# Kernel optimization log

Measured on AMD Instinct MI355X. Metric: run time of the kernel, lower is better.

Reference implementation:

```python
import jax, jax.numpy as jnp
import numpy as np

OUT, IN = 14336, 4096          # Llama FFN up-projection
N = OUT * IN                   # total quantized elements
NB = N // 64                   # NF4 blocks (blocksize 64)
NG = N // 256                  # double-quant groups (group size 256)
B = 32                         # batch rows


def setup_inputs() -> dict:
    key = jax.random.key(0)
    ks = jax.random.split(key, 7)
    x = jax.random.normal(ks[0], (B, IN), dtype=jnp.float16)
    # packed bytes: two 4-bit nibbles per byte (values 0..255)
    packed = jax.random.randint(ks[1], (N // 2,), 0, 256, dtype=jnp.int32)
    absmax = jax.random.uniform(ks[2], (NB,), dtype=jnp.float32)                     # per-block absmax
    code = jax.random.uniform(ks[3], (NB,), jnp.float32, minval=0.5, maxval=1.5)     # per-block code scale
    offset = jax.random.uniform(ks[4], (NB,), jnp.float32, minval=0.0, maxval=8.0)   # per-block offset
    g_absmax = jax.random.uniform(ks[5], (NG,), jnp.float32, minval=0.5, maxval=1.5) # nested (state2) absmax
    g_code = jax.random.uniform(ks[6], (NG,), jnp.float32, minval=0.5, maxval=1.5)   # nested (state2) code
    return {"x": x, "packed": packed, "absmax": absmax, "code": code,
            "offset": offset, "g_absmax": g_absmax, "g_code": g_code}


def _dequantize_nf4(packed, absmax, code, offset, g_absmax, g_code):
    # Unpack nibbles: even element = low nibble (byte & 15), odd = high nibble (byte >> 4)
    low = packed & 15
    high = packed >> 4
    nib = jnp.stack([low, high], axis=-1).reshape(-1).astype(jnp.float32)  # [N]
    # Nested (double) dequantization scales, matching the Triton kernel:
    # combined_scale = (absmax / code) * (g_absmax / g_code)
    block_scale = absmax / code                      # [NB]
    group_scale = g_absmax / g_code                  # [NG]
    cs_block = block_scale * jnp.repeat(group_scale, 64 * 4 // 64)  # each group spans 4 blocks -> [NB]
    cs = jnp.repeat(cs_block, 64)                    # per-element combined scale [N]
    off = jnp.repeat(offset, 64)                     # per-element offset [N]
    # dequantized = nibble * cs - offset * cs (as written in the kernel), stored as fp16
    deq = (nib * cs - off * cs).astype(jnp.float16)
    return deq.reshape(OUT, IN)


def reference(x, packed, absmax, code, offset, g_absmax, g_code):
    W = _dequantize_nf4(packed, absmax, code, offset, g_absmax, g_code)  # [OUT, IN] fp16
    return x @ W.T                                                        # [B, OUT] fp16
```

## Files before the change

### kernel.cpp

```cpp
#include <hip/hip_runtime.h>
#include <hip/hip_bf16.h>


#define OUT_D 14336
#define IN_D  4096
#define B_D   32
#define KSPLIT 8
#define KRANGE (IN_D / KSPLIT)
#define KC 64
#define CHUNKS (KRANGE / KC)
#define NB (OUT_D * IN_D / 64)
#define SZ_X (B_D * IN_D)

typedef __attribute__((ext_vector_type(4))) float f32x4;
typedef __attribute__((ext_vector_type(2))) float f32x2;
typedef __attribute__((ext_vector_type(4))) int   i32x4;
typedef __bf16 bf16x8 __attribute__((ext_vector_type(8)));
using u16 = unsigned short;

typedef const __attribute__((address_space(1))) void* gas1_t;
typedef __attribute__((address_space(3))) void* las3_t;

__device__ __forceinline__ void gll16(const void* g, void* l) {
    __builtin_amdgcn_global_load_lds((gas1_t)g, (las3_t)l, 16, 0, 0);
}

__global__ __launch_bounds__(256) void pre_kernel(
    const float* __restrict__ x,
    const float* __restrict__ absmax, const float* __restrict__ code,
    const float* __restrict__ offset,
    const float* __restrict__ g_absmax, const float* __restrict__ g_code,
    u16* __restrict__ xb, f32x2* __restrict__ csn)
{
    const int i = blockIdx.x * 256 + threadIdx.x;
    float am = absmax[i], cd = code[i], of = offset[i];
    float ga = g_absmax[i >> 2], gc = g_code[i >> 2];
    float cs = (am * ga) / (cd * gc);
    f32x2 v; v.x = cs; v.y = -of * cs;
    csn[i] = v;
    if (i < SZ_X) {
        __bf16 h = (__bf16)x[i];
        xb[i] = __builtin_bit_cast(u16, h);
    }
}

__global__ __launch_bounds__(256, 3) void nf4_main(
    const u16* __restrict__ xb,
    const int* __restrict__ packed,
    const f32x2* __restrict__ csn,
    float* __restrict__ part)
{
    __shared__ u16 xs[B_D][512];
    __shared__ int wb[3][32][32];

    const int t      = threadIdx.x;
    const int o_base = blockIdx.x * 32;
    const int kz     = blockIdx.y;

    const int wave = t >> 6, lane = t & 63;
    const int m_base = (wave & 1) * 16, n_base = (wave >> 1) * 16;
    const int frow = lane & 15, q = lane >> 4;
    const int rown = n_base + frow;
    const int rowa = m_base + frow;

    #pragma unroll
    for (int j = 0; j < 8; ++j) {
        int slot = t + j * 256;
        int r = slot >> 6, c = slot & 63;
        bf16x8 v = *reinterpret_cast<const bf16x8*>(xb + r * IN_D + kz * KRANGE + c * 8);
        *reinterpret_cast<bf16x8*>(&xs[r][(c ^ (r & 7)) * 8]) = v;
    }

    f32x4 scp[4];
    {
        const f32x4* sp = reinterpret_cast<const f32x4*>(
            csn + (o_base + rown) * 64 + kz * CHUNKS);
        scp[0] = sp[0]; scp[1] = sp[1]; scp[2] = sp[2]; scp[3] = sp[3];
    }
    __builtin_amdgcn_sched_barrier(0);

    const int srow = t >> 3;
    const int scol = (t & 7) ^ (srow & 7);
    const int* gsrc = packed + (o_base + srow) * (IN_D / 2)
                             + kz * (KRANGE / 2) + scol * 4;

    gll16(gsrc + 0 * 32, &wb[0][wave * 8][0]);
    gll16(gsrc + 1 * 32, &wb[1][wave * 8][0]);

    f32x4 acc = {0.f, 0.f, 0.f, 0.f};

    #pragma unroll
    for (int C = 0; C < CHUNKS; ++C) {
        if (C == 0)               asm volatile("s_waitcnt vmcnt(1) lgkmcnt(0)" ::: "memory");
        else if (C < CHUNKS - 1)  asm volatile("s_waitcnt vmcnt(1)" ::: "memory");
        else                      asm volatile("s_waitcnt vmcnt(0)" ::: "memory");
        __builtin_amdgcn_s_barrier();
        __builtin_amdgcn_sched_barrier(0);

        if (C + 2 < CHUNKS)
            gll16(gsrc + (C + 2) * 32, &wb[(C + 2) % 3][wave * 8][0]);

        const int buf = C % 3;
        const float cs  = scp[C >> 1][(C & 1) * 2];
        const float noc = scp[C >> 1][(C & 1) * 2 + 1];

        #pragma unroll
        for (int s = 0; s < 2; ++s) {
            i32x4 braw = *reinterpret_cast<const i32x4*>(
                &wb[buf][rown][(((s * 4 + q) ^ (rown & 7)) * 4)]);
            int ca = C * 8 + s * 4 + q;
            bf16x8 a = *reinterpret_cast<const bf16x8*>(
                &xs[rowa][(ca ^ (rowa & 7)) * 8]);
            bf16x8 b;
            #pragma unroll
            for (int w = 0; w < 4; ++w) {
                int ww = braw[w];
                b[2 * w]     = (__bf16)fmaf((float)(ww & 15),        cs, noc);
                b[2 * w + 1] = (__bf16)fmaf((float)((ww >> 4) & 15), cs, noc);
            }
            acc = __builtin_amdgcn_mfma_f32_16x16x32_bf16(a, b, acc, 0, 0, 0);
        }
    }

    float* pp = part + (size_t)kz * (B_D * OUT_D);
    const int oc = o_base + n_base + frow;
    const int r0 = m_base + q * 4;
    #pragma unroll
    for (int i = 0; i < 4; ++i)
        pp[(r0 + i) * OUT_D + oc] = acc[i];
}

__global__ __launch_bounds__(256) void reduce_kernel(
    const float* __restrict__ part, float* __restrict__ out)
{
    const int i = (blockIdx.x * 256 + threadIdx.x) * 4;
    f32x4 s = *reinterpret_cast<const f32x4*>(part + i);
    #pragma unroll
    for (int k = 1; k < KSPLIT; ++k) {
        f32x4 v = *reinterpret_cast<const f32x4*>(
            part + (size_t)k * (B_D * OUT_D) + i);
        s[0] += v[0]; s[1] += v[1]; s[2] += v[2]; s[3] += v[3];
    }
    *reinterpret_cast<f32x4*>(out + i) = s;
}

extern "C" void kernel_launch(void* const* d_in, const int* in_sizes, int n_in,
                              void* d_out, int out_size, void* d_ws, size_t ws_size,
                              hipStream_t stream) {
    const void* px = nullptr;
    const void* ppk = nullptr;
    const void* trio[3] = {nullptr, nullptr, nullptr};
    const void* pair[2] = {nullptr, nullptr};
    int ntrio = 0, npair = 0;
    const int SZ_PK  = OUT_D * (IN_D / 2);
    const int SZ_NB  = NB;
    const int SZ_NG  = OUT_D * (IN_D / 256);
    for (int i = 0; i < n_in; ++i) {
        int s = in_sizes[i];
        if (s == SZ_X) px = d_in[i];
        else if (s == SZ_PK) ppk = d_in[i];
        else if (s == SZ_NB) { if (ntrio < 3) trio[ntrio++] = d_in[i]; }
        else if (s == SZ_NG) { if (npair < 2) pair[npair++] = d_in[i]; }
    }
    if (!px || !ppk || ntrio != 3 || npair != 2) {
        px = d_in[0]; ppk = d_in[1];
        trio[0] = d_in[2]; trio[1] = d_in[3]; trio[2] = d_in[4];
        pair[0] = d_in[5]; pair[1] = d_in[6];
    }

    char* ws = (char*)d_ws;
    u16*   xb   = (u16*)ws;
    f32x2* csn  = (f32x2*)(ws + 262144);
    float* part = (float*)(ws + 262144 + (size_t)NB * 8);

    pre_kernel<<<dim3(NB / 256), dim3(256), 0, stream>>>(
        (const float*)px,
        (const float*)trio[0], (const float*)trio[1], (const float*)trio[2],
        (const float*)pair[0], (const float*)pair[1],
        xb, csn);

    nf4_main<<<dim3(OUT_D / 32, KSPLIT), dim3(256), 0, stream>>>(
        xb, (const int*)ppk, csn, part);

    reduce_kernel<<<dim3(B_D * OUT_D / 4 / 256), dim3(256), 0, stream>>>(
        part, (float*)d_out);
}
```

Before: 47.91 us.

## Reduce K-split to 2 with atomic output and larger weight chunks

Lowers the K-split from 8 to 2 and raises the chunk size to 256, so each block streams bigger weight tiles through a triple-buffered LDS pipeline. The x operand now comes straight from global/L2 into registers rather than being staged in LDS. The partial-sum buffer and the separate reduce kernel are removed in favour of a memset plus float atomicAdd into the output. This cuts the partial-buffer write and read traffic and one launch. In exchange the grid drops to 896 blocks, which may leave the GPU underfilled, and the result can vary with atomic ordering.

```diff
diff --git a/kernel.cpp b/kernel.cpp
--- a/kernel.cpp
+++ b/kernel.cpp
@@ -5,9 +5,9 @@
 #define OUT_D 14336
 #define IN_D  4096
 #define B_D   32
-#define KSPLIT 8
+#define KSPLIT 2
 #define KRANGE (IN_D / KSPLIT)
-#define KC 64
+#define KC 256
 #define CHUNKS (KRANGE / KC)
 #define NB (OUT_D * IN_D / 64)
 #define SZ_X (B_D * IN_D)
@@ -44,14 +44,13 @@
     }
 }
 
-__global__ __launch_bounds__(256, 3) void nf4_main(
+__global__ __launch_bounds__(256) void nf4_main(
     const u16* __restrict__ xb,
     const int* __restrict__ packed,
     const f32x2* __restrict__ csn,
-    float* __restrict__ part)
+    float* __restrict__ out)
 {
-    __shared__ u16 xs[B_D][512];
-    __shared__ int wb[3][32][32];
+    __shared__ int wlds[3][32 * 128];
 
     const int t      = threadIdx.x;
     const int o_base = blockIdx.x * 32;
@@ -60,57 +59,60 @@
     const int wave = t >> 6, lane = t & 63;
     const int m_base = (wave & 1) * 16, n_base = (wave >> 1) * 16;
     const int frow = lane & 15, q = lane >> 4;
-    const int rown = n_base + frow;
-    const int rowa = m_base + frow;
 
+    const int* gsrc[4];
     #pragma unroll
-    for (int j = 0; j < 8; ++j) {
-        int slot = t + j * 256;
-        int r = slot >> 6, c = slot & 63;
-        bf16x8 v = *reinterpret_cast<const bf16x8*>(xb + r * IN_D + kz * KRANGE + c * 8);
-        *reinterpret_cast<bf16x8*>(&xs[r][(c ^ (r & 7)) * 8]) = v;
+    for (int j = 0; j < 4; ++j) {
+        int g  = wave * 4 + j;
+        int lr = 2 * g + (lane >> 5);
+        int su = (lane & 31) ^ (lr & 7);
+        gsrc[j] = packed + (size_t)(o_base + lr) * (IN_D / 2)
+                         + kz * (KRANGE / 2) + su * 4;
     }
 
-    f32x4 scp[4];
-    {
-        const f32x4* sp = reinterpret_cast<const f32x4*>(
-            csn + (o_base + rown) * 64 + kz * CHUNKS);
-        scp[0] = sp[0]; scp[1] = sp[1]; scp[2] = sp[2]; scp[3] = sp[3];
-    }
-    __builtin_amdgcn_sched_barrier(0);
-
-    const int srow = t >> 3;
-    const int scol = (t & 7) ^ (srow & 7);
-    const int* gsrc = packed + (o_base + srow) * (IN_D / 2)
-                             + kz * (KRANGE / 2) + scol * 4;
-
-    gll16(gsrc + 0 * 32, &wb[0][wave * 8][0]);
-    gll16(gsrc + 1 * 32, &wb[1][wave * 8][0]);
+    const int lrB   = n_base + frow;
+    const int rowA  = m_base + frow;
+    const u16*  abase = xb + rowA * IN_D + kz * KRANGE;
+    const f32x2* cbase = csn + (size_t)(o_base + lrB) * 64 + kz * (KRANGE / 64);
 
     f32x4 acc = {0.f, 0.f, 0.f, 0.f};
 
     #pragma unroll
+    for (int j = 0; j < 4; ++j) gll16(gsrc[j] + 0 * 128, &wlds[0][(wave * 4 + j) * 256]);
+    #pragma unroll
+    for (int j = 0; j < 4; ++j) gll16(gsrc[j] + 1 * 128, &wlds[1][(wave * 4 + j) * 256]);
+
+    #pragma unroll
     for (int C = 0; C < CHUNKS; ++C) {
-        if (C == 0)               asm volatile("s_waitcnt vmcnt(1) lgkmcnt(0)" ::: "memory");
-        else if (C < CHUNKS - 1)  asm volatile("s_waitcnt vmcnt(1)" ::: "memory");
-        else                      asm volatile("s_waitcnt vmcnt(0)" ::: "memory");
+        if (C < CHUNKS - 1) asm volatile("s_waitcnt vmcnt(4)" ::: "memory");
+        else                asm volatile("s_waitcnt vmcnt(0)" ::: "memory");
         __builtin_amdgcn_s_barrier();
         __builtin_amdgcn_sched_barrier(0);
 
-        if (C + 2 < CHUNKS)
-            gll16(gsrc + (C + 2) * 32, &wb[(C + 2) % 3][wave * 8][0]);
+        bf16x8 a[8];
+        #pragma unroll
+        for (int ks = 0; ks < 8; ++ks)
+            a[ks] = *reinterpret_cast<const bf16x8*>(abase + C * KC + ks * 32 + q * 8);
+        f32x4 sc0 = *reinterpret_cast<const f32x4*>(cbase + C * 4);
+        f32x4 sc1 = *reinterpret_cast<const f32x4*>(cbase + C * 4 + 2);
+        __builtin_amdgcn_sched_barrier(0);
+
+        if (C + 2 < CHUNKS) {
+            #pragma unroll
+            for (int j = 0; j < 4; ++j)
+                gll16(gsrc[j] + (C + 2) * 128, &wlds[(C + 2) % 3][(wave * 4 + j) * 256]);
+        }
+        __builtin_amdgcn_sched_barrier(0);
 
         const int buf = C % 3;
-        const float cs  = scp[C >> 1][(C & 1) * 2];
-        const float noc = scp[C >> 1][(C & 1) * 2 + 1];
-
         #pragma unroll
-        for (int s = 0; s < 2; ++s) {
+        for (int ks = 0; ks < 8; ++ks) {
             i32x4 braw = *reinterpret_cast<const i32x4*>(
-                &wb[buf][rown][(((s * 4 + q) ^ (rown & 7)) * 4)]);
-            int ca = C * 8 + s * 4 + q;
-            bf16x8 a = *reinterpret_cast<const bf16x8*>(
-                &xs[rowa][(ca ^ (rowa & 7)) * 8]);
+                &wlds[buf][lrB * 128 + (((ks * 4 + q) ^ (lrB & 7)) * 4)]);
+            const float cs  = (ks < 4) ? ((ks < 2) ? sc0[0] : sc0[2])
+                                       : ((ks < 6) ? sc1[0] : sc1[2]);
+            const float noc = (ks < 4) ? ((ks < 2) ? sc0[1] : sc0[3])
+                                       : ((ks < 6) ? sc1[1] : sc1[3]);
             bf16x8 b;
             #pragma unroll
             for (int w = 0; w < 4; ++w) {
@@ -118,30 +120,15 @@
                 b[2 * w]     = (__bf16)fmaf((float)(ww & 15),        cs, noc);
                 b[2 * w + 1] = (__bf16)fmaf((float)((ww >> 4) & 15), cs, noc);
             }
-            acc = __builtin_amdgcn_mfma_f32_16x16x32_bf16(a, b, acc, 0, 0, 0);
+            acc = __builtin_amdgcn_mfma_f32_16x16x32_bf16(a[ks], b, acc, 0, 0, 0);
         }
     }
 
-    float* pp = part + (size_t)kz * (B_D * OUT_D);
     const int oc = o_base + n_base + frow;
     const int r0 = m_base + q * 4;
     #pragma unroll
     for (int i = 0; i < 4; ++i)
-        pp[(r0 + i) * OUT_D + oc] = acc[i];
-}
-
-__global__ __launch_bounds__(256) void reduce_kernel(
-    const float* __restrict__ part, float* __restrict__ out)
-{
-    const int i = (blockIdx.x * 256 + threadIdx.x) * 4;
-    f32x4 s = *reinterpret_cast<const f32x4*>(part + i);
-    #pragma unroll
-    for (int k = 1; k < KSPLIT; ++k) {
-        f32x4 v = *reinterpret_cast<const f32x4*>(
-            part + (size_t)k * (B_D * OUT_D) + i);
-        s[0] += v[0]; s[1] += v[1]; s[2] += v[2]; s[3] += v[3];
-    }
-    *reinterpret_cast<f32x4*>(out + i) = s;
+        atomicAdd(&out[(r0 + i) * OUT_D + oc], acc[i]);
 }
 
 extern "C" void kernel_launch(void* const* d_in, const int* in_sizes, int n_in,
@@ -153,13 +140,12 @@
     const void* pair[2] = {nullptr, nullptr};
     int ntrio = 0, npair = 0;
     const int SZ_PK  = OUT_D * (IN_D / 2);
-    const int SZ_NB  = NB;
     const int SZ_NG  = OUT_D * (IN_D / 256);
     for (int i = 0; i < n_in; ++i) {
         int s = in_sizes[i];
         if (s == SZ_X) px = d_in[i];
         else if (s == SZ_PK) ppk = d_in[i];
-        else if (s == SZ_NB) { if (ntrio < 3) trio[ntrio++] = d_in[i]; }
+        else if (s == NB) { if (ntrio < 3) trio[ntrio++] = d_in[i]; }
         else if (s == SZ_NG) { if (npair < 2) pair[npair++] = d_in[i]; }
     }
     if (!px || !ppk || ntrio != 3 || npair != 2) {
@@ -169,9 +155,8 @@
     }
 
     char* ws = (char*)d_ws;
-    u16*   xb   = (u16*)ws;
-    f32x2* csn  = (f32x2*)(ws + 262144);
-    float* part = (float*)(ws + 262144 + (size_t)NB * 8);
+    u16*   xb  = (u16*)ws;
+    f32x2* csn = (f32x2*)(ws + 262144);
 
     pre_kernel<<<dim3(NB / 256), dim3(256), 0, stream>>>(
         (const float*)px,
@@ -179,9 +164,8 @@
         (const float*)pair[0], (const float*)pair[1],
         xb, csn);
 
+    hipMemsetAsync(d_out, 0, (size_t)out_size * sizeof(float), stream);
+
     nf4_main<<<dim3(OUT_D / 32, KSPLIT), dim3(256), 0, stream>>>(
-        xb, (const int*)ppk, csn, part);
-
-    reduce_kernel<<<dim3(B_D * OUT_D / 4 / 256), dim3(256), 0, stream>>>(
-        part, (float*)d_out);
+        xb, (const int*)ppk, csn, (float*)d_out);
 }
```

Result: slower. 62.09 us, median of 2 (+29.6%).
